# Optimization experiments

Measured on AMD Instinct MI355X. Metric: run time of the kernel, lower is better.

The kernel has to match this reference:

```python
import jax, jax.numpy as jnp
import numpy as np

RADIUS = 0.2        # init arg
MAX_SAMPLES = 64    # init arg


def setup_inputs() -> dict:
    key = jax.random.key(0)
    k1, k2 = jax.random.split(key)
    B, N, M = 8, 16384, 1024
    pt_coordinates = jax.random.uniform(k1, (B, 3, N), dtype=jnp.float32)
    centroids = jax.random.uniform(k2, (B, 3, M), dtype=jnp.float32)
    return {"pt_coordinates": pt_coordinates, "centroids": centroids}


def reference(pt_coordinates, centroids):
    """Ball query: for each centroid, indices of up to MAX_SAMPLES points
    within RADIUS. Slots beyond the found neighbors are padded with the
    first neighbor's index (standard PointNet++ semantics).
    Returns group_idx: [B, M, MAX_SAMPLES] int32.
    """
    B, _, N = pt_coordinates.shape
    M = centroids.shape[2]
    # squared pairwise distances via ||c||^2 + ||p||^2 - 2 c.p  -> [B, M, N]
    p2 = jnp.sum(pt_coordinates * pt_coordinates, axis=1)          # [B, N]
    c2 = jnp.sum(centroids * centroids, axis=1)                    # [B, M]
    cp = jnp.einsum('bdm,bdn->bmn', centroids, pt_coordinates)     # [B, M, N]
    d2 = c2[:, :, None] + p2[:, None, :] - 2.0 * cp                # [B, M, N]
    r2 = jnp.float32(RADIUS * RADIUS)
    # candidate index where inside ball, sentinel N where outside
    idx = jnp.where(d2 <= r2, jnp.arange(N, dtype=jnp.int32)[None, None, :],
                    jnp.int32(N))                                   # [B, M, N]
    # first MAX_SAMPLES in-radius indices (ascending; sentinels sort last)
    idx_k = jnp.sort(idx, axis=-1)[..., :MAX_SAMPLES]               # [B, M, K]
    first = idx_k[..., :1]
    # if a centroid has zero neighbors, fall back to index 0 (CUDA init value)
    first = jnp.where(first == N, jnp.int32(0), first)
    group_idx = jnp.where(idx_k == N, first, idx_k)
    return group_idx
```

## Files before the change

kernel.cpp:

```cpp
#include <hip/hip_runtime.h>


#define BQ_N 16384
#define BQ_M 1024
#define BQ_K 64
#define BQ_R2 0.04f

__global__ __launch_bounds__(256) void BallPointQuery_kernel(
    const float* __restrict__ pts,
    const float* __restrict__ cents,
    int* __restrict__ out)
{
    const int N = BQ_N, M = BQ_M, K = BQ_K;
    const int lane = threadIdx.x & 63;
    const int cid  = (blockIdx.x << 2) + (threadIdx.x >> 6);
    const int b = cid >> 10;
    const int m = cid & (M - 1);

    const float* p = pts   + (size_t)b * 3 * N;
    const float* c = cents + (size_t)b * 3 * M;
    const float cx = c[m];
    const float cy = c[M + m];
    const float cz = c[2 * M + m];

    const float c2 = __fadd_rn(__fadd_rn(__fmul_rn(cx, cx), __fmul_rn(cy, cy)),
                               __fmul_rn(cz, cz));

    int* o = out + (size_t)cid * K;

    int count = 0;
    int first = 0;

    for (int base = 0; base < N && count < K; base += 256) {
        float px[4], py[4], pz[4];
        #pragma unroll
        for (int j = 0; j < 4; ++j) {
            const int i = base + 64 * j + lane;
            px[j] = p[i];
            py[j] = p[N + i];
            pz[j] = p[2 * N + i];
        }

        #pragma unroll
        for (int j = 0; j < 4; ++j) {
            const float p2 = __fadd_rn(
                __fadd_rn(__fmul_rn(px[j], px[j]), __fmul_rn(py[j], py[j])),
                __fmul_rn(pz[j], pz[j]));
            float cp = __fmul_rn(cx, px[j]);
            cp = __fmaf_rn(cy, py[j], cp);
            cp = __fmaf_rn(cz, pz[j], cp);
            const float d2 = __fsub_rn(__fadd_rn(c2, p2), __fmul_rn(2.0f, cp));

            const unsigned long long mask = __ballot(d2 <= BQ_R2);
            if (mask) {
                const int i = base + 64 * j + lane;
                if (count == 0) first = base + 64 * j + __builtin_ctzll(mask);
                const bool hit = (mask >> lane) & 1ull;
                const int slot = count + __popcll(mask & ((1ull << lane) - 1ull));
                if (hit && slot < K) o[slot] = i;
                count += __popcll(mask);
                if (count >= K) break;
            }
        }
    }

    const int cnt = count < K ? count : K;
    if (lane >= cnt) o[lane] = first;
}

extern "C" void kernel_launch(void* const* d_in, const int* in_sizes, int n_in,
                              void* d_out, int out_size, void* d_ws, size_t ws_size,
                              hipStream_t stream) {
    const float* pts   = (const float*)d_in[0];
    const float* cents = (const float*)d_in[1];
    int* out = (int*)d_out;

    BallPointQuery_kernel<<<8192 / 4, 256, 0, stream>>>(pts, cents, out);
}
```

Baseline: 80.98 us.

## Vectorize point loads as float4 with register prefetch and batched ballots

Each lane now loads four consecutive points per coordinate as a float4 and prefetches the next 256-point chunk while the current one is processed. The four per-point hit bits are combined into four ballots, and output slots come from one prefix count per chunk. This aims to cut load instruction count, hide global memory latency, and reduce branching per ballot, at the cost of more registers and an extra prefetch after the early exit.

```diff
diff --git a/kernel.cpp b/kernel.cpp
--- a/kernel.cpp
+++ b/kernel.cpp
@@ -28,40 +28,71 @@
 
     int* o = out + (size_t)cid * K;
 
+    const float4* px4 = (const float4*)(p);
+    const float4* py4 = (const float4*)(p + N);
+    const float4* pz4 = (const float4*)(p + 2 * N);
+
     int count = 0;
     int first = 0;
 
-    for (int base = 0; base < N && count < K; base += 256) {
-        float px[4], py[4], pz[4];
-        #pragma unroll
-        for (int j = 0; j < 4; ++j) {
-            const int i = base + 64 * j + lane;
-            px[j] = p[i];
-            py[j] = p[N + i];
-            pz[j] = p[2 * N + i];
+    float4 X = px4[lane], Y = py4[lane], Z = pz4[lane];
+
+    for (int base = 0; base < N; base += 256) {
+        float4 Xn, Yn, Zn;
+        const int nb = base + 256;
+        if (nb < N) {
+            const int q = (nb >> 2) + lane;
+            Xn = px4[q]; Yn = py4[q]; Zn = pz4[q];
         }
 
+        const float xs[4] = {X.x, X.y, X.z, X.w};
+        const float ys[4] = {Y.x, Y.y, Y.z, Y.w};
+        const float zs[4] = {Z.x, Z.y, Z.z, Z.w};
+        unsigned nib = 0;
         #pragma unroll
-        for (int j = 0; j < 4; ++j) {
+        for (int k = 0; k < 4; ++k) {
             const float p2 = __fadd_rn(
-                __fadd_rn(__fmul_rn(px[j], px[j]), __fmul_rn(py[j], py[j])),
-                __fmul_rn(pz[j], pz[j]));
-            float cp = __fmul_rn(cx, px[j]);
-            cp = __fmaf_rn(cy, py[j], cp);
-            cp = __fmaf_rn(cz, pz[j], cp);
+                __fadd_rn(__fmul_rn(xs[k], xs[k]), __fmul_rn(ys[k], ys[k])),
+                __fmul_rn(zs[k], zs[k]));
+            float cp = __fmul_rn(cx, xs[k]);
+            cp = __fmaf_rn(cy, ys[k], cp);
+            cp = __fmaf_rn(cz, zs[k], cp);
             const float d2 = __fsub_rn(__fadd_rn(c2, p2), __fmul_rn(2.0f, cp));
+            nib |= (d2 <= BQ_R2 ? 1u : 0u) << k;
+        }
 
-            const unsigned long long mask = __ballot(d2 <= BQ_R2);
-            if (mask) {
-                const int i = base + 64 * j + lane;
-                if (count == 0) first = base + 64 * j + __builtin_ctzll(mask);
-                const bool hit = (mask >> lane) & 1ull;
-                const int slot = count + __popcll(mask & ((1ull << lane) - 1ull));
-                if (hit && slot < K) o[slot] = i;
-                count += __popcll(mask);
-                if (count >= K) break;
+        const unsigned long long m0 = __ballot((nib >> 0) & 1u);
+        const unsigned long long m1 = __ballot((nib >> 1) & 1u);
+        const unsigned long long m2 = __ballot((nib >> 2) & 1u);
+        const unsigned long long m3 = __ballot((nib >> 3) & 1u);
+        const unsigned long long any = m0 | m1 | m2 | m3;
+
+        if (any) {
+            if (count == 0) {
+                const int l0 = __builtin_ctzll(any);
+                const unsigned n0 =
+                      (unsigned)((m0 >> l0) & 1ull)
+                    | ((unsigned)((m1 >> l0) & 1ull) << 1)
+                    | ((unsigned)((m2 >> l0) & 1ull) << 2)
+                    | ((unsigned)((m3 >> l0) & 1ull) << 3);
+                first = base + 4 * l0 + __builtin_ctz(n0);
             }
+            const unsigned long long below = (1ull << lane) - 1ull;
+            int s = count + __popcll(m0 & below) + __popcll(m1 & below)
+                          + __popcll(m2 & below) + __popcll(m3 & below);
+            const int idx0 = base + 4 * lane;
+            #pragma unroll
+            for (int k = 0; k < 4; ++k) {
+                if ((nib >> k) & 1u) {
+                    if (s < K) o[s] = idx0 + k;
+                    ++s;
+                }
+            }
+            count += __popcll(m0) + __popcll(m1) + __popcll(m2) + __popcll(m3);
+            if (count >= K) break;
         }
+
+        X = Xn; Y = Yn; Z = Zn;
     }
 
     const int cnt = count < K ? count : K;
```

Measured after the change: 82.07 us. Within noise of the previous version (+1.3%).
